# Kernel optimization log

Hardware: AMD Instinct MI355X
Metric: run time of the kernel (lower is better)

The kernel has to match this reference:

```python
import jax, jax.numpy as jnp
import numpy as np

NUM_INPUTS = 2048
NUM_GATES = 8192
BATCH = 2048


def setup_inputs() -> dict:
    key = jax.random.key(0)
    k1, k2, k3 = jax.random.split(key, 3)
    x = jax.random.uniform(k1, (BATCH, NUM_INPUTS), dtype=jnp.float32)
    w = jax.random.normal(k2, (16, NUM_GATES), dtype=jnp.float32)
    c = jax.random.normal(k3, (NUM_INPUTS, NUM_GATES, 2), dtype=jnp.float32)
    return {"x": x, "w": w, "c": c}


def reference(x, w, c):
    num_inputs, num_gates, _ = c.shape
    # softmax over input wires -> soft connection matrix [I, 2G]
    connections = jax.nn.softmax(c, axis=0).reshape(num_inputs, num_gates * 2)
    y = (x @ connections).reshape(x.shape[0], num_gates, 2)  # [B, G, 2]
    A = y[:, :, 0]  # [B, G]
    B = y[:, :, 1]  # [B, G]
    AB = A * B
    ones = jnp.ones_like(A)
    zeros = jnp.zeros_like(A)
    g7 = A + B - AB
    g6 = g7 - AB
    # 16 soft logic gates, stacked on a leading axis: [16, B, G]
    gates = jnp.stack([
        zeros, AB, A - AB, A, B - AB, B, g6, g7,
        ones - g7, ones - g6, ones - B, ones - (B - AB),
        ones - A, ones - (A - AB), ones - AB, ones,
    ], axis=0)
    weights = jax.nn.softmax(w, axis=0)  # [16, G]
    # weighted combine over gate types -> [B, G]
    out = jnp.einsum('kbg,kg->bg', gates, weights)
    return out
```

## Files before the change

### kernel.cpp

```cpp
#include <hip/hip_runtime.h>
#include <hip/hip_bf16.h>
#include <stdint.h>

#define BATCH   2048
#define NIN     2048
#define NGATES  8192
#define NCOL    16384

typedef short s16x8 __attribute__((ext_vector_type(8)));
typedef float f32x4 __attribute__((ext_vector_type(4)));

__device__ __forceinline__ void gload_lds16(const void* g, void* l) {
  __builtin_amdgcn_global_load_lds(
      (const __attribute__((address_space(1))) void*)g,
      (__attribute__((address_space(3))) void*)l,
      16, 0, 0);
}

__device__ __forceinline__ unsigned short f2bf(float f) {
  __hip_bfloat16 h = __float2bfloat16(f);
  return __builtin_bit_cast(unsigned short, h);
}
__device__ __forceinline__ float bf2f(unsigned int u) {
  return __bfloat162float(__builtin_bit_cast(__hip_bfloat16,
                                             (unsigned short)(u & 0xffff)));
}

__global__ __launch_bounds__(256) void gate_coeff_k(const float* __restrict__ w,
                                                    float4* __restrict__ coeff) {
  const int g = blockIdx.x * 256 + threadIdx.x;
  float e[16];
  float s = 0.f;
#pragma unroll
  for (int k = 0; k < 16; ++k) { e[k] = __expf(w[k * NGATES + g]); s += e[k]; }
  const float inv = 1.0f / s;
#pragma unroll
  for (int k = 0; k < 16; ++k) e[k] *= inv;
  const float P0 = e[8] + e[9] + e[10] + e[11] + e[12] + e[13] + e[14] + e[15];
  const float P1 = e[2] + e[3] + e[6] + e[7] - e[8] - e[9] - e[12] - e[13];
  const float P2 = e[4] + e[5] + e[6] + e[7] - e[8] - e[9] - e[10] - e[11];
  const float P3 = e[1] - e[2] - e[4] - 2.f * e[6] - e[7] + e[8] + 2.f * e[9]
                 + e[11] + e[13] - e[14];
  coeff[g] = make_float4(P0, P1, P2, P3);
}

__global__ __launch_bounds__(256) void cvt_x_k(const float4* __restrict__ x,
                                               ushort4* __restrict__ xb) {
  const int i = blockIdx.x * 256 + threadIdx.x;
  float4 v = x[i];
  ushort4 h;
  h.x = f2bf(v.x); h.y = f2bf(v.y); h.z = f2bf(v.z); h.w = f2bf(v.w);
  xb[i] = h;
}

__global__ __launch_bounds__(256) void softmax_t_k(const float* __restrict__ c,
                                                   unsigned short* __restrict__ bT,
                                                   float* __restrict__ psums) {
  __shared__ float red[16][68];
  const int t = threadIdx.x;
  const int ng = (t & 15) * 4;
  const int kg = t >> 4;
  const int n0 = blockIdx.x * 64;
  const int q  = blockIdx.y;
  const float* cb = c + (size_t)n0 + ng;
  float s0 = 0.f, s1 = 0.f, s2 = 0.f, s3 = 0.f;

  float4 v[8], nv[8];
  {
    const int r0 = q * 512 + kg * 8;
#pragma unroll
    for (int d = 0; d < 8; ++d)
      v[d] = *(const float4*)&cb[(size_t)(r0 + d) * NCOL];
  }
  for (int it = 0; it < 4; ++it) {
    if (it < 3) {
      const int r1 = q * 512 + (it + 1) * 128 + kg * 8;
#pragma unroll
      for (int d = 0; d < 8; ++d)
        nv[d] = *(const float4*)&cb[(size_t)(r1 + d) * NCOL];
    }
    unsigned int u[4][4];
#pragma unroll
    for (int d2 = 0; d2 < 4; ++d2) {
      float4 e0 = v[2 * d2], e1 = v[2 * d2 + 1];
      unsigned int a0 = f2bf(__expf(e0.x)), b0 = f2bf(__expf(e1.x));
      unsigned int a1 = f2bf(__expf(e0.y)), b1 = f2bf(__expf(e1.y));
      unsigned int a2 = f2bf(__expf(e0.z)), b2 = f2bf(__expf(e1.z));
      unsigned int a3 = f2bf(__expf(e0.w)), b3 = f2bf(__expf(e1.w));
      s0 += bf2f(a0) + bf2f(b0);
      s1 += bf2f(a1) + bf2f(b1);
      s2 += bf2f(a2) + bf2f(b2);
      s3 += bf2f(a3) + bf2f(b3);
      u[0][d2] = a0 | (b0 << 16);
      u[1][d2] = a1 | (b1 << 16);
      u[2][d2] = a2 | (b2 << 16);
      u[3][d2] = a3 | (b3 << 16);
    }
    const int i0 = q * 512 + it * 128 + kg * 8;
#pragma unroll
    for (int j = 0; j < 4; ++j) {
      uint4 pk = make_uint4(u[j][0], u[j][1], u[j][2], u[j][3]);
      *(uint4*)&bT[(size_t)(n0 + ng + j) * NIN + i0] = pk;
    }
    if (it < 3) {
#pragma unroll
      for (int d = 0; d < 8; ++d) v[d] = nv[d];
    }
  }
  red[kg][ng + 0] = s0;
  red[kg][ng + 1] = s1;
  red[kg][ng + 2] = s2;
  red[kg][ng + 3] = s3;
  __syncthreads();
  if (t < 64) {
    float tot = 0.f;
#pragma unroll
    for (int k2 = 0; k2 < 16; ++k2) tot += red[k2][t];
    psums[(size_t)q * NCOL + n0 + t] = tot;
  }
}

__global__ __launch_bounds__(256) void inv_k(const float* __restrict__ psums,
                                             float* __restrict__ invs) {
  const int n = blockIdx.x * 256 + threadIdx.x;
  invs[n] = 1.0f / (psums[n] + psums[NCOL + n] + psums[2 * NCOL + n] +
                    psums[3 * NCOL + n]);
}

#define MFMA_B16(a, b, c) __builtin_amdgcn_mfma_f32_16x16x32_bf16(a, b, c, 0, 0, 0)

__global__ __launch_bounds__(512, 2) void gemm_gate_k(
    const unsigned short* __restrict__ xb,
    const unsigned short* __restrict__ bT,
    const float* __restrict__ invs,
    const float4* __restrict__ coeff,
    float* __restrict__ out) {
  extern __shared__ char smem[];
  constexpr int NT = 32;

  const int t  = threadIdx.x;
  const int l  = t & 63;
  const int w  = t >> 6;
  const int wm = w >> 2;
  const int wn = w & 3;
  const int fr = l & 15;
  const int cq = l >> 4;

  const int bid = blockIdx.x;
  const int xcd = bid & 7;
  const int loc = bid >> 3;
  const int m0  = (loc & 7) * 256;
  const int g0  = (xcd * 8 + (loc >> 3)) * 128;

  uint32_t offA[2][2], offB[2][2];
#pragma unroll
  for (int r = 0; r < 2; ++r) {
    const int idx = r * 512 + t;
    const int lr  = idx >> 3;
    const int ch  = (idx & 7) ^ (lr & 7);
    const int rA  = (lr & 63) + ((lr >> 6) << 7);
    offA[0][r] = (uint32_t)(m0 + rA) * NIN + ch * 8;
    offA[1][r] = offA[0][r] + (uint32_t)64 * NIN;
    offB[0][r] = (uint32_t)(2 * (g0 + lr)) * NIN + ch * 8;
    offB[1][r] = offB[0][r] + NIN;
  }

  auto issueA = [&](int u, int tt) {
    char* d = smem + ((tt & 1) << 16) + (u << 14) + t * 16;
    gload_lds16(xb + offA[u][0] + tt * 64, d);
    gload_lds16(xb + offA[u][1] + tt * 64, d + 8192);
  };
  auto issueB = [&](int u, int tt) {
    char* d = smem + ((tt & 1) << 16) + ((2 + u) << 14) + t * 16;
    gload_lds16(bT + offB[u][0] + tt * 64, d);
    gload_lds16(bT + offB[u][1] + tt * 64, d + 8192);
  };

  const int aob = (wm * 64 + fr) * 128;
  const int bob = 32768 + (wn * 32 + fr) * 128;
  const int sx0 = ((cq)     ^ (fr & 7)) * 16;
  const int sx1 = ((cq + 4) ^ (fr & 7)) * 16;

  f32x4 acc[8][4] = {};
  s16x8 af[8];
  s16x8 bfr[8];

  issueA(0, 0); issueA(1, 0); issueB(0, 0); issueB(1, 0);
  issueA(0, 1); issueB(0, 1); issueB(1, 1);
  asm volatile("s_waitcnt vmcnt(6)" ::: "memory");
  asm volatile("s_barrier" ::: "memory");

  for (int kt = 0; kt < NT; ++kt) {
    char* rb = smem + ((kt & 1) << 16);

#pragma unroll
    for (int i = 0; i < 4; ++i) {
      af[i * 2 + 0] = *(const s16x8*)(rb + aob + i * 2048 + sx0);
      af[i * 2 + 1] = *(const s16x8*)(rb + aob + i * 2048 + sx1);
    }
#pragma unroll
    for (int j = 0; j < 2; ++j) {
      bfr[j * 2 + 0] = *(const s16x8*)(rb + bob + j * 2048 + sx0);
      bfr[j * 2 + 1] = *(const s16x8*)(rb + bob + j * 2048 + sx1);
    }
    if (kt + 1 < NT) issueA(1, kt + 1);
    asm volatile("s_barrier" ::: "memory");
    asm volatile("s_waitcnt lgkmcnt(0)" ::: "memory");
    __builtin_amdgcn_s_setprio(1);
#pragma unroll
    for (int i = 0; i < 4; ++i)
#pragma unroll
      for (int j = 0; j < 2; ++j) {
        acc[i][j] = MFMA_B16(af[i * 2 + 0], bfr[j * 2 + 0], acc[i][j]);
        acc[i][j] = MFMA_B16(af[i * 2 + 1], bfr[j * 2 + 1], acc[i][j]);
      }
    __builtin_amdgcn_s_setprio(0);
    asm volatile("s_barrier" ::: "memory");

#pragma unroll
    for (int j = 0; j < 2; ++j) {
      bfr[4 + j * 2 + 0] = *(const s16x8*)(rb + bob + 16384 + j * 2048 + sx0);
      bfr[4 + j * 2 + 1] = *(const s16x8*)(rb + bob + 16384 + j * 2048 + sx1);
    }
    if (kt + 2 < NT) issueA(0, kt + 2);
    asm volatile("s_barrier" ::: "memory");
    asm volatile("s_waitcnt lgkmcnt(0)" ::: "memory");
    __builtin_amdgcn_s_setprio(1);
#pragma unroll
    for (int i = 0; i < 4; ++i)
#pragma unroll
      for (int j = 0; j < 2; ++j) {
        acc[i][2 + j] = MFMA_B16(af[i * 2 + 0], bfr[4 + j * 2 + 0], acc[i][2 + j]);
        acc[i][2 + j] = MFMA_B16(af[i * 2 + 1], bfr[4 + j * 2 + 1], acc[i][2 + j]);
      }
    __builtin_amdgcn_s_setprio(0);
    asm volatile("s_barrier" ::: "memory");

#pragma unroll
    for (int i = 0; i < 4; ++i) {
      af[i * 2 + 0] = *(const s16x8*)(rb + 16384 + aob + i * 2048 + sx0);
      af[i * 2 + 1] = *(const s16x8*)(rb + 16384 + aob + i * 2048 + sx1);
    }
    if (kt + 2 < NT) issueB(0, kt + 2);
    asm volatile("s_barrier" ::: "memory");
    asm volatile("s_waitcnt lgkmcnt(0)" ::: "memory");
    __builtin_amdgcn_s_setprio(1);
#pragma unroll
    for (int i = 0; i < 4; ++i)
#pragma unroll
      for (int j = 0; j < 2; ++j) {
        acc[4 + i][2 + j] = MFMA_B16(af[i * 2 + 0], bfr[4 + j * 2 + 0], acc[4 + i][2 + j]);
        acc[4 + i][2 + j] = MFMA_B16(af[i * 2 + 1], bfr[4 + j * 2 + 1], acc[4 + i][2 + j]);
      }
    __builtin_amdgcn_s_setprio(0);
    asm volatile("s_barrier" ::: "memory");

    if (kt + 2 < NT) issueB(1, kt + 2);
    asm volatile("s_barrier" ::: "memory");
    asm volatile("s_waitcnt lgkmcnt(0)" ::: "memory");
    __builtin_amdgcn_s_setprio(1);
#pragma unroll
    for (int i = 0; i < 4; ++i)
#pragma unroll
      for (int j = 0; j < 2; ++j) {
        acc[4 + i][j] = MFMA_B16(af[i * 2 + 0], bfr[j * 2 + 0], acc[4 + i][j]);
        acc[4 + i][j] = MFMA_B16(af[i * 2 + 1], bfr[j * 2 + 1], acc[4 + i][j]);
      }
    __builtin_amdgcn_s_setprio(0);
    if (kt < NT - 2) {
      asm volatile("s_waitcnt vmcnt(6)" ::: "memory");
    } else {
      asm volatile("s_waitcnt vmcnt(0)" ::: "memory");
    }
    asm volatile("s_barrier" ::: "memory");
  }

#pragma unroll
  for (int j = 0; j < 2; ++j) {
    const int gate = g0 + wn * 32 + j * 16 + fr;
    const float2 iv = *(const float2*)&invs[2 * gate];
    const float4 P  = coeff[gate];
#pragma unroll
    for (int i = 0; i < 8; ++i) {
#pragma unroll
      for (int r = 0; r < 4; ++r) {
        const float A = acc[i][j][r]     * iv.x;
        const float B = acc[i][j + 2][r] * iv.y;
        const float res = P.x + P.y * A + P.z * B + P.w * A * B;
        const int m = m0 + wm * 128 + i * 16 + cq * 4 + r;
        out[(size_t)m * NGATES + gate] = res;
      }
    }
  }
}

extern "C" void kernel_launch(void* const* d_in, const int* in_sizes, int n_in,
                              void* d_out, int out_size, void* d_ws,
                              size_t ws_size, hipStream_t stream) {
  const float* x = (const float*)d_in[0];
  const float* w = (const float*)d_in[1];
  const float* c = (const float*)d_in[2];
  float* out = (float*)d_out;
  char* ws = (char*)d_ws;

  unsigned short* xb   = (unsigned short*)(ws);
  unsigned short* bT   = (unsigned short*)(ws + 8388608);
  float*          invs = (float*)(ws + 75497472);
  float4*         cf   = (float4*)(ws + 75563008);
  float*          ps   = (float*)(ws + 75694080);

  static bool attr_done = false;
  if (!attr_done) {
    (void)hipFuncSetAttribute(reinterpret_cast<const void*>(gemm_gate_k),
                              hipFuncAttributeMaxDynamicSharedMemorySize,
                              131072);
    attr_done = true;
  }

  gate_coeff_k<<<NGATES / 256, 256, 0, stream>>>(w, cf);
  cvt_x_k<<<(BATCH * NIN / 4) / 256, 256, 0, stream>>>((const float4*)x,
                                                       (ushort4*)xb);
  dim3 sg(NCOL / 64, 4);
  softmax_t_k<<<sg, 256, 0, stream>>>(c, bT, ps);
  inv_k<<<NCOL / 256, 256, 0, stream>>>(ps, invs);
  gemm_gate_k<<<512, 512, 131072, stream>>>(xb, bT, invs, cf, out);
}
```

Measured before the change: 352.6 us.

## Stage softmax transpose through swizzled LDS tile and merge small prep kernels

Result: no change. 348.9 us (-1.0%).

```diff
diff --git a/kernel.cpp b/kernel.cpp
--- a/kernel.cpp
+++ b/kernel.cpp
@@ -26,55 +26,60 @@
                                              (unsigned short)(u & 0xffff)));
 }
 
-__global__ __launch_bounds__(256) void gate_coeff_k(const float* __restrict__ w,
-                                                    float4* __restrict__ coeff) {
-  const int g = blockIdx.x * 256 + threadIdx.x;
-  float e[16];
-  float s = 0.f;
-#pragma unroll
-  for (int k = 0; k < 16; ++k) { e[k] = __expf(w[k * NGATES + g]); s += e[k]; }
-  const float inv = 1.0f / s;
-#pragma unroll
-  for (int k = 0; k < 16; ++k) e[k] *= inv;
-  const float P0 = e[8] + e[9] + e[10] + e[11] + e[12] + e[13] + e[14] + e[15];
-  const float P1 = e[2] + e[3] + e[6] + e[7] - e[8] - e[9] - e[12] - e[13];
-  const float P2 = e[4] + e[5] + e[6] + e[7] - e[8] - e[9] - e[10] - e[11];
-  const float P3 = e[1] - e[2] - e[4] - 2.f * e[6] - e[7] + e[8] + 2.f * e[9]
-                 + e[11] + e[13] - e[14];
-  coeff[g] = make_float4(P0, P1, P2, P3);
-}
-
-__global__ __launch_bounds__(256) void cvt_x_k(const float4* __restrict__ x,
-                                               ushort4* __restrict__ xb) {
-  const int i = blockIdx.x * 256 + threadIdx.x;
-  float4 v = x[i];
-  ushort4 h;
-  h.x = f2bf(v.x); h.y = f2bf(v.y); h.z = f2bf(v.z); h.w = f2bf(v.w);
-  xb[i] = h;
+__global__ __launch_bounds__(256) void pre_k(const float4* __restrict__ x,
+                                             ushort4* __restrict__ xb,
+                                             const float* __restrict__ w,
+                                             float4* __restrict__ coeff) {
+  const int b = blockIdx.x;
+  const int t = threadIdx.x;
+  if (b < 4096) {
+    const int i = b * 256 + t;
+    float4 v = x[i];
+    ushort4 h;
+    h.x = f2bf(v.x); h.y = f2bf(v.y); h.z = f2bf(v.z); h.w = f2bf(v.w);
+    xb[i] = h;
+  } else {
+    const int g = (b - 4096) * 256 + t;
+    float e[16];
+    float s = 0.f;
+#pragma unroll
+    for (int k = 0; k < 16; ++k) { e[k] = __expf(w[k * NGATES + g]); s += e[k]; }
+    const float inv = 1.0f / s;
+#pragma unroll
+    for (int k = 0; k < 16; ++k) e[k] *= inv;
+    const float P0 = e[8] + e[9] + e[10] + e[11] + e[12] + e[13] + e[14] + e[15];
+    const float P1 = e[2] + e[3] + e[6] + e[7] - e[8] - e[9] - e[12] - e[13];
+    const float P2 = e[4] + e[5] + e[6] + e[7] - e[8] - e[9] - e[10] - e[11];
+    const float P3 = e[1] - e[2] - e[4] - 2.f * e[6] - e[7] + e[8] + 2.f * e[9]
+                   + e[11] + e[13] - e[14];
+    coeff[g] = make_float4(P0, P1, P2, P3);
+  }
 }
 
 __global__ __launch_bounds__(256) void softmax_t_k(const float* __restrict__ c,
                                                    unsigned short* __restrict__ bT,
                                                    float* __restrict__ psums) {
-  __shared__ float red[16][68];
-  const int t = threadIdx.x;
-  const int ng = (t & 15) * 4;
-  const int kg = t >> 4;
-  const int n0 = blockIdx.x * 64;
-  const int q  = blockIdx.y;
+  extern __shared__ char sm4[];
+  char*  tile = sm4;
+  float* red  = (float*)(sm4 + 65536);
+  const int t  = threadIdx.x;
+  const int ng = (t & 127) * 4;
+  const int kg = t >> 7;
+  const int n0 = blockIdx.x * 512;
+  const int k0 = blockIdx.y * 64;
   const float* cb = c + (size_t)n0 + ng;
   float s0 = 0.f, s1 = 0.f, s2 = 0.f, s3 = 0.f;
 
   float4 v[8], nv[8];
   {
-    const int r0 = q * 512 + kg * 8;
+    const int r0 = k0 + kg * 8;
 #pragma unroll
     for (int d = 0; d < 8; ++d)
       v[d] = *(const float4*)&cb[(size_t)(r0 + d) * NCOL];
   }
   for (int it = 0; it < 4; ++it) {
     if (it < 3) {
-      const int r1 = q * 512 + (it + 1) * 128 + kg * 8;
+      const int r1 = k0 + (it + 1) * 16 + kg * 8;
 #pragma unroll
       for (int d = 0; d < 8; ++d)
         nv[d] = *(const float4*)&cb[(size_t)(r1 + d) * NCOL];
@@ -96,35 +101,50 @@
       u[2][d2] = a2 | (b2 << 16);
       u[3][d2] = a3 | (b3 << 16);
     }
-    const int i0 = q * 512 + it * 128 + kg * 8;
+    const int chunk = it * 2 + kg;
+    const int sw    = (chunk ^ (t & 7)) * 16;
 #pragma unroll
     for (int j = 0; j < 4; ++j) {
       uint4 pk = make_uint4(u[j][0], u[j][1], u[j][2], u[j][3]);
-      *(uint4*)&bT[(size_t)(n0 + ng + j) * NIN + i0] = pk;
+      *(uint4*)&tile[(ng + j) * 128 + sw] = pk;
     }
     if (it < 3) {
 #pragma unroll
       for (int d = 0; d < 8; ++d) v[d] = nv[d];
     }
   }
-  red[kg][ng + 0] = s0;
-  red[kg][ng + 1] = s1;
-  red[kg][ng + 2] = s2;
-  red[kg][ng + 3] = s3;
+  red[kg * 516 + ng + 0] = s0;
+  red[kg * 516 + ng + 1] = s1;
+  red[kg * 516 + ng + 2] = s2;
+  red[kg * 516 + ng + 3] = s3;
   __syncthreads();
-  if (t < 64) {
-    float tot = 0.f;
-#pragma unroll
-    for (int k2 = 0; k2 < 16; ++k2) tot += red[k2][t];
-    psums[(size_t)q * NCOL + n0 + t] = tot;
+
+  {
+    const int rsub = t >> 3;
+    const int ch   = t & 7;
+#pragma unroll
+    for (int p = 0; p < 16; ++p) {
+      const int row = p * 32 + rsub;
+      const int sw  = (ch ^ ((row >> 2) & 7)) * 16;
+      uint4 vv = *(const uint4*)&tile[row * 128 + sw];
+      *(uint4*)&bT[(size_t)(n0 + row) * NIN + k0 + ch * 8] = vv;
+    }
+  }
+  {
+    const int c0 = 2 * t;
+    const float2 tot = make_float2(
+        red[c0] + red[516 + c0], red[c0 + 1] + red[516 + c0 + 1]);
+    *(float2*)&psums[(size_t)blockIdx.y * NCOL + n0 + c0] = tot;
   }
 }
 
 __global__ __launch_bounds__(256) void inv_k(const float* __restrict__ psums,
                                              float* __restrict__ invs) {
   const int n = blockIdx.x * 256 + threadIdx.x;
-  invs[n] = 1.0f / (psums[n] + psums[NCOL + n] + psums[2 * NCOL + n] +
-                    psums[3 * NCOL + n]);
+  float s = 0.f;
+#pragma unroll
+  for (int q = 0; q < 32; ++q) s += psums[(size_t)q * NCOL + n];
+  invs[n] = 1.0f / s;
 }
 
 #define MFMA_B16(a, b, c) __builtin_amdgcn_mfma_f32_16x16x32_bf16(a, b, c, 0, 0, 0)
@@ -165,15 +185,15 @@
     offB[1][r] = offB[0][r] + NIN;
   }
 
-  auto issueA = [&](int u, int tt) {
-    char* d = smem + ((tt & 1) << 16) + (u << 14) + t * 16;
-    gload_lds16(xb + offA[u][0] + tt * 64, d);
-    gload_lds16(xb + offA[u][1] + tt * 64, d + 8192);
+  auto issueA = [&](int u, int kt) {
+    char* d = smem + ((kt & 1) << 16) + (u << 14) + t * 16;
+    gload_lds16(xb + offA[u][0] + kt * 64, d);
+    gload_lds16(xb + offA[u][1] + kt * 64, d + 8192);
   };
-  auto issueB = [&](int u, int tt) {
-    char* d = smem + ((tt & 1) << 16) + ((2 + u) << 14) + t * 16;
-    gload_lds16(bT + offB[u][0] + tt * 64, d);
-    gload_lds16(bT + offB[u][1] + tt * 64, d + 8192);
+  auto issueB = [&](int u, int kt) {
+    char* d = smem + ((kt & 1) << 16) + ((2 + u) << 14) + t * 16;
+    gload_lds16(bT + offB[u][0] + kt * 64, d);
+    gload_lds16(bT + offB[u][1] + kt * 64, d + 8192);
   };
 
   const int aob = (wm * 64 + fr) * 128;
@@ -303,25 +323,26 @@
   float* out = (float*)d_out;
   char* ws = (char*)d_ws;
 
-  unsigned short* xb   = (unsigned short*)(ws);
-  unsigned short* bT   = (unsigned short*)(ws + 8388608);
-  float*          invs = (float*)(ws + 75497472);
-  float4*         cf   = (float4*)(ws + 75563008);
-  float*          ps   = (float*)(ws + 75694080);
+  unsigned short* xb  = (unsigned short*)(ws);
+  unsigned short* bT  = (unsigned short*)(ws + 8388608);
+  float*          psv = (float*)(ws + 75497472);
+  float*          ivv = (float*)(ws + 77594624);
+  float4*         cf  = (float4*)(ws + 77660160);
 
   static bool attr_done = false;
   if (!attr_done) {
     (void)hipFuncSetAttribute(reinterpret_cast<const void*>(gemm_gate_k),
                               hipFuncAttributeMaxDynamicSharedMemorySize,
                               131072);
+    (void)hipFuncSetAttribute(reinterpret_cast<const void*>(softmax_t_k),
+                              hipFuncAttributeMaxDynamicSharedMemorySize,
+                              69664);
     attr_done = true;
   }
 
-  gate_coeff_k<<<NGATES / 256, 256, 0, stream>>>(w, cf);
-  cvt_x_k<<<(BATCH * NIN / 4) / 256, 256, 0, stream>>>((const float4*)x,
-                                                       (ushort4*)xb);
-  dim3 sg(NCOL / 64, 4);
-  softmax_t_k<<<sg, 256, 0, stream>>>(c, bT, ps);
-  inv_k<<<NCOL / 256, 256, 0, stream>>>(ps, invs);
-  gemm_gate_k<<<512, 512, 131072, stream>>>(xb, bT, invs, cf, out);
-}
+  pre_k<<<4128, 256, 0, stream>>>((const float4*)x, (ushort4*)xb, w, cf);
+  dim3 sg(NCOL / 512, NIN / 64);
+  softmax_t_k<<<sg, 256, 69664, stream>>>(c, bT, psv);
+  inv_k<<<NCOL / 256, 256, 0, stream>>>(psv, ivv);
+  gemm_gate_k<<<512, 512, 131072, stream>>>(xb, bT, ivv, cf, out);
+}
```
